# Performance work log

Measured on AMD Instinct MI355X. Metric: run time of the kernel, lower is better.

## Reference

```python
import jax, jax.numpy as jnp
import numpy as np
import math

H = 16
D_MODEL = 1024
D_K = D_MODEL // H
B = 4
S = 2048


def setup_inputs() -> dict:
    key = jax.random.key(0)
    ks = jax.random.split(key, 11)
    s_in = 1.0 / math.sqrt(D_MODEL)
    inp = {
        "query": jax.random.normal(ks[0], (B, S, D_MODEL), dtype=jnp.float32),
        "key_": jax.random.normal(ks[1], (B, S, D_MODEL), dtype=jnp.float32),
        "value": jax.random.normal(ks[2], (B, S, D_MODEL), dtype=jnp.float32),
        # stacked per-head projection weights: [h, d_model, d_k]
        "Wq": jax.random.uniform(ks[3], (H, D_MODEL, D_K), jnp.float32, -s_in, s_in),
        "bq": jax.random.uniform(ks[4], (H, D_K), jnp.float32, -s_in, s_in),
        "Wk": jax.random.uniform(ks[5], (H, D_MODEL, D_K), jnp.float32, -s_in, s_in),
        "bk": jax.random.uniform(ks[6], (H, D_K), jnp.float32, -s_in, s_in),
        "Wv": jax.random.uniform(ks[7], (H, D_MODEL, D_K), jnp.float32, -s_in, s_in),
        "bv": jax.random.uniform(ks[8], (H, D_K), jnp.float32, -s_in, s_in),
        "Wo": jax.random.uniform(ks[9], (D_MODEL, D_MODEL), jnp.float32, -s_in, s_in),
        "bo": jax.random.uniform(ks[10], (D_MODEL,), jnp.float32, -s_in, s_in),
    }
    return inp


def reference(query, key_, value, Wq, bq, Wk, bk, Wv, bv, Wo, bo):
    # Per-head projections, batched over heads: [b,s,m] x [h,m,k] -> [b,h,s,k]
    q = jnp.einsum("bsm,hmk->bhsk", query, Wq) + bq[None, :, None, :]
    k = jnp.einsum("bsm,hmk->bhsk", key_, Wk) + bk[None, :, None, :]
    v = jnp.einsum("bsm,hmk->bhsk", value, Wv) + bv[None, :, None, :]
    # scores: q @ k^T -> [b,h,Sq,Sk]
    scores = jnp.einsum("bhqk,bhsk->bhqs", q, k) / jnp.sqrt(jnp.float32(D_K))
    # NOTE: original code softmaxes over dim=1 of the per-head [N,Sq,Sk]
    # tensor, i.e. the QUERY axis (axis=2 here). Mask has no effect
    # (masked_fill result is discarded in the source), so it is omitted.
    attn = jax.nn.softmax(scores, axis=2)
    ctx = jnp.einsum("bhqs,bhsk->bhqk", attn, v)  # [b,h,Sq,d_k]
    # concat heads along last dim (head-major order matches torch.cat)
    ctx = jnp.transpose(ctx, (0, 2, 1, 3)).reshape(B, S, D_MODEL)
    out = ctx @ Wo.T + bo  # final_W; dropout = identity (eval mode)
    return out
```

## Files before the change

kernel.cpp:

```cpp
#include <hip/hip_runtime.h>


#define DEV __device__ __forceinline__

typedef __bf16 bf16x8 __attribute__((ext_vector_type(8)));
typedef float  f32x4  __attribute__((ext_vector_type(4)));

DEV unsigned short f2bf(float f) {
    __bf16 h = (__bf16)f;
    return __builtin_bit_cast(unsigned short, h);
}

DEV bf16x8 ldfrag(const unsigned short* p) {
    return *reinterpret_cast<const bf16x8*>(p);
}

DEV float fast_exp2(float x) {
#if __has_builtin(__builtin_amdgcn_exp2f)
    return __builtin_amdgcn_exp2f(x);
#else
    return exp2f(x);
#endif
}

DEV void gld16(const unsigned short* g, unsigned short* l) {
    __builtin_amdgcn_global_load_lds(
        (__attribute__((address_space(1))) void*)g,
        (__attribute__((address_space(3))) void*)l, 16, 0, 0);
}

#define MFMA(a,b,c) __builtin_amdgcn_mfma_f32_16x16x32_bf16((a),(b),(c),0,0,0)

#define QSCALE 0.18033688011112042f

__global__ __launch_bounds__(256) void wprep(const float* __restrict__ Wq,
                                             const float* __restrict__ Wk,
                                             const float* __restrict__ Wv,
                                             const float* __restrict__ Wo,
                                             unsigned short* __restrict__ Wt,
                                             unsigned short* __restrict__ Wot) {
    int idx = blockIdx.x * 256 + threadIdx.x;
    int which = blockIdx.y;
    if (which == 3) { Wot[idx] = f2bf(Wo[idx]); return; }
    const float* W = (which == 0) ? Wq : (which == 1) ? Wk : Wv;
    int n = idx >> 10, m = idx & 1023;
    int h = n >> 6, k = n & 63;
    Wt[(size_t)which * 1048576 + idx] = f2bf(W[h * 65536 + m * 64 + k]);
}

__global__ __launch_bounds__(256) void xprep(const float* __restrict__ X,
                                             unsigned short* __restrict__ Xb) {
    int idx = (blockIdx.x * 256 + threadIdx.x) * 4;
    float4 f = *(const float4*)&X[idx];
    ushort4 o;
    o.x = f2bf(f.x); o.y = f2bf(f.y); o.z = f2bf(f.z); o.w = f2bf(f.w);
    *(ushort4*)&Xb[idx] = o;
}

__global__ __launch_bounds__(256) void proj_gemm(
        const unsigned short* __restrict__ Xb, const unsigned short* __restrict__ Bt,
        const float* __restrict__ bias, unsigned short* __restrict__ O,
        unsigned short* __restrict__ Vt, int z) {
    const int tid = threadIdx.x;
    const int bm = blockIdx.x, bn = blockIdx.y;

    __shared__ __align__(16) unsigned short As[128 * 32];
    __shared__ __align__(16) unsigned short Bs[128 * 32];

    const int lane = tid & 63, wid = tid >> 6;
    const int l16 = lane & 15, quad = lane >> 4;
    const int wm = wid & 1, wn = wid >> 1;

    const unsigned short* ga =
        Xb + (size_t)(bm * 128 + wid * 32 + (lane >> 2)) * 1024 + (lane & 3) * 8;
    const unsigned short* gb =
        Bt + (size_t)(bn * 128 + wid * 32 + (lane >> 2)) * 1024 + (lane & 3) * 8;
    unsigned short* la = &As[wid * 32 * 32];
    unsigned short* lb = &Bs[wid * 32 * 32];

    f32x4 acc[4][4] = {};
    for (int kt = 0; kt < 32; ++kt) {
        __syncthreads();
        const int k0 = kt * 32;
        gld16(ga + k0, la);
        gld16(ga + k0 + 16 * 1024, la + 16 * 32);
        gld16(gb + k0, lb);
        gld16(gb + k0 + 16 * 1024, lb + 16 * 32);
        __syncthreads();
        bf16x8 af[4], bfr[4];
#pragma unroll
        for (int mi = 0; mi < 4; ++mi)
            af[mi] = ldfrag(&As[(wm * 64 + mi * 16 + l16) * 32 + quad * 8]);
#pragma unroll
        for (int ni = 0; ni < 4; ++ni)
            bfr[ni] = ldfrag(&Bs[(wn * 64 + ni * 16 + l16) * 32 + quad * 8]);
#pragma unroll
        for (int mi = 0; mi < 4; ++mi)
#pragma unroll
            for (int ni = 0; ni < 4; ++ni)
                acc[mi][ni] = MFMA(af[mi], bfr[ni], acc[mi][ni]);
    }

    if (z == 2) {
#pragma unroll
        for (int mi = 0; mi < 4; ++mi) {
            int row0 = bm * 128 + wm * 64 + mi * 16 + quad * 4;
            int b = row0 >> 11, s0 = row0 & 2047;
#pragma unroll
            for (int ni = 0; ni < 4; ++ni) {
                int col = bn * 128 + wn * 64 + ni * 16 + l16;
                int h = col >> 6, k = col & 63;
                float bi = bias[col];
                ushort4 o;
                o.x = f2bf(acc[mi][ni][0] + bi);
                o.y = f2bf(acc[mi][ni][1] + bi);
                o.z = f2bf(acc[mi][ni][2] + bi);
                o.w = f2bf(acc[mi][ni][3] + bi);
                *(ushort4*)&Vt[(size_t)((b * 16 + h) * 64 + k) * 2048 + s0] = o;
            }
        }
    } else {
#pragma unroll
        for (int mi = 0; mi < 4; ++mi)
#pragma unroll
            for (int ni = 0; ni < 4; ++ni)
#pragma unroll
                for (int r = 0; r < 4; ++r) {
                    int row = bm * 128 + wm * 64 + mi * 16 + quad * 4 + r;
                    int col = bn * 128 + wn * 64 + ni * 16 + l16;
                    float v = acc[mi][ni][r] + bias[col];
                    if (z == 0) v *= QSCALE;
                    int b = row >> 11, s = row & 2047;
                    int h = col >> 6, k = col & 63;
                    O[(size_t)((b * 16 + h) * 2048 + s) * 64 + k] = f2bf(v);
                }
    }
}

__global__ __launch_bounds__(256) void colsum_vscale(
        const unsigned short* __restrict__ Qh, const unsigned short* __restrict__ Kh,
        unsigned short* __restrict__ Vt) {
    const int tid = threadIdx.x;
    const int st = blockIdx.x, bh = blockIdx.y;
    const unsigned short* Qb = Qh + (size_t)bh * 2048 * 64;
    const unsigned short* Kb = Kh + (size_t)bh * 2048 * 64;

    __shared__ __align__(16) unsigned short Qs[2][128 * 64];
    __shared__ float Dtmp[2][128];
    __shared__ float Dsh[128];

    const int lane = tid & 63, wid = tid >> 6;
    const int l16 = lane & 15, quad = lane >> 4;
    const int wm = wid & 1, wn = wid >> 1;
    const int l7 = l16 & 7;

    bf16x8 kf[2][4];
#pragma unroll
    for (int ks = 0; ks < 2; ++ks)
#pragma unroll
        for (int ni = 0; ni < 4; ++ni)
            kf[ks][ni] = ldfrag(&Kb[(size_t)(st * 128 + wn * 64 + ni * 16 + l16) * 64 +
                                    ks * 32 + quad * 8]);

    const unsigned short* gq = Qb + (size_t)(wid * 32 + (lane >> 3)) * 64 +
                               ((lane & 7) ^ (lane >> 3)) * 8;

#pragma unroll
    for (int gi = 0; gi < 4; ++gi)
        gld16(gq + (size_t)gi * 8 * 64, &Qs[0][(wid * 32 + gi * 8) * 64]);

    float psum[4] = {0.f, 0.f, 0.f, 0.f};
    for (int it = 0; it < 16; ++it) {
        const int buf = it & 1;
        __syncthreads();
        if (it < 15) {
            const size_t q1 = (size_t)(it + 1) * 128;
#pragma unroll
            for (int gi = 0; gi < 4; ++gi)
                gld16(gq + (q1 + gi * 8) * 64, &Qs[buf ^ 1][(wid * 32 + gi * 8) * 64]);
        }
        f32x4 acc[4][4] = {};
#pragma unroll
        for (int ks = 0; ks < 2; ++ks) {
            bf16x8 af[4];
#pragma unroll
            for (int mi = 0; mi < 4; ++mi)
                af[mi] = ldfrag(&Qs[buf][(wm * 64 + mi * 16 + l16) * 64 +
                                         (((ks * 4 + quad) ^ l7) * 8)]);
            __builtin_amdgcn_s_setprio(1);
#pragma unroll
            for (int mi = 0; mi < 4; ++mi)
#pragma unroll
                for (int ni = 0; ni < 4; ++ni)
                    acc[mi][ni] = MFMA(af[mi], kf[ks][ni], acc[mi][ni]);
            __builtin_amdgcn_s_setprio(0);
        }
#pragma unroll
        for (int ni = 0; ni < 4; ++ni) {
            float d = 0.f;
#pragma unroll
            for (int mi = 0; mi < 4; ++mi)
#pragma unroll
                for (int r = 0; r < 4; ++r)
                    d += fast_exp2(acc[mi][ni][r]);
            psum[ni] += d;
        }
    }
#pragma unroll
    for (int ni = 0; ni < 4; ++ni) {
        float v = psum[ni];
        v += __shfl_xor(v, 16, 64);
        v += __shfl_xor(v, 32, 64);
        if (quad == 0) Dtmp[wm][wn * 64 + ni * 16 + l16] = v;
    }
    __syncthreads();
    if (tid < 128) Dsh[tid] = 1.0f / (Dtmp[0][tid] + Dtmp[1][tid]);
    __syncthreads();

    const int k = tid >> 2, c = tid & 3;
    unsigned short* vrow = Vt + ((size_t)bh * 64 + k) * 2048 + st * 128 + c * 32;
#pragma unroll
    for (int j = 0; j < 4; ++j) {
        bf16x8 v = *(const bf16x8*)&vrow[j * 8];
        bf16x8 o;
#pragma unroll
        for (int e = 0; e < 8; ++e)
            o[e] = (__bf16)((float)v[e] * Dsh[c * 32 + j * 8 + e]);
        *(bf16x8*)&vrow[j * 8] = o;
    }
}

__global__ __launch_bounds__(256) void attnpv(const unsigned short* __restrict__ Qh,
                                              const unsigned short* __restrict__ Kh,
                                              const unsigned short* __restrict__ Vn,
                                              unsigned short* __restrict__ Ctx) {
    const int tid = threadIdx.x;
    const int qt = blockIdx.x, bh = blockIdx.y;
    const int b = bh >> 4, h = bh & 15;
    const unsigned short* Qb = Qh + (size_t)bh * 2048 * 64;
    const unsigned short* Kb = Kh + (size_t)bh * 2048 * 64;
    const unsigned short* Vb = Vn + (size_t)bh * 64 * 2048;

    __shared__ __align__(16) unsigned char smem[36864];
    unsigned short* Ks = (unsigned short*)smem;
    unsigned short* Vs = (unsigned short*)(smem + 16384);
    unsigned short* Pw = (unsigned short*)(smem + 32768) + (tid >> 6) * 512;

    const int lane = tid & 63, wid = tid >> 6;
    const int l16 = lane & 15, quad = lane >> 4;
    const int wq = wid & 1, ws = wid >> 1;
    const int l7 = l16 & 7;
    const int ph = (l16 >> 1) & 7;
    const int pql = l16 & 1;

    bf16x8 qf[2][4];
#pragma unroll
    for (int ks = 0; ks < 2; ++ks)
#pragma unroll
        for (int nj = 0; nj < 4; ++nj)
            qf[ks][nj] = ldfrag(&Qb[(size_t)(qt * 128 + wq * 64 + nj * 16 + l16) * 64 +
                                    ks * 32 + quad * 8]);

    const int half = wid & 1;
    const int sr8 = lane >> 3;
    const int sg = ((lane & 7) ^ sr8) * 8;
    const unsigned short* gk = Kb + (size_t)(half * 32 + sr8) * 64 + sg;
    const unsigned short* gv = Vb + (size_t)(half * 32 + sr8) * 2048 + sg;

    if (wid < 2) {
#pragma unroll
        for (int gi = 0; gi < 4; ++gi)
            gld16(gk + (size_t)gi * 8 * 64, &Ks[(half * 32 + gi * 8) * 64]);
    } else {
#pragma unroll
        for (int gi = 0; gi < 4; ++gi)
            gld16(gv + (size_t)gi * 8 * 2048, &Vs[(half * 32 + gi * 8) * 64]);
    }

    f32x4 cacc[4][4] = {};
    for (int it = 0; it < 32; ++it) {
        const int pb = it & 1;
        __syncthreads();

        if (it < 31) {
            const size_t s1 = (size_t)(it + 1) * 64;
            if (wid < 2) {
#pragma unroll
                for (int gi = 0; gi < 4; ++gi)
                    gld16(gk + (s1 + gi * 8) * 64,
                          &Ks[(pb ^ 1) * 4096 + (half * 32 + gi * 8) * 64]);
            } else {
#pragma unroll
                for (int gi = 0; gi < 4; ++gi)
                    gld16(gv + (size_t)gi * 8 * 2048 + s1,
                          &Vs[(pb ^ 1) * 4096 + (half * 32 + gi * 8) * 64]);
            }
        }

        bf16x8 kf[2][2];
#pragma unroll
        for (int mi = 0; mi < 2; ++mi)
#pragma unroll
            for (int ks = 0; ks < 2; ++ks)
                kf[mi][ks] = ldfrag(&Ks[pb * 4096 + (ws * 32 + mi * 16 + l16) * 64 +
                                        (((ks * 4 + quad) ^ l7) * 8)]);
        f32x4 sacc[2][4] = {};
        __builtin_amdgcn_s_setprio(1);
#pragma unroll
        for (int ks = 0; ks < 2; ++ks)
#pragma unroll
            for (int mi = 0; mi < 2; ++mi)
#pragma unroll
                for (int nj = 0; nj < 4; ++nj)
                    sacc[mi][nj] = MFMA(kf[mi][ks], qf[ks][nj], sacc[mi][nj]);
        __builtin_amdgcn_s_setprio(0);

        bf16x8 vf[4];
#pragma unroll
        for (int mi = 0; mi < 4; ++mi)
            vf[mi] = ldfrag(&Vs[pb * 4096 + (mi * 16 + l16) * 64 +
                                (((ws * 4 + quad) ^ l7) * 8)]);

#pragma unroll
        for (int nj = 0; nj < 4; ++nj) {
#pragma unroll
            for (int mi = 0; mi < 2; ++mi) {
                const int G = pql * 4 + mi * 2 + (quad >> 1);
                const int po = ((G ^ ph) * 8) + (quad & 1) * 4;
                ushort4 p;
                p.x = f2bf(fast_exp2(sacc[mi][nj][0]));
                p.y = f2bf(fast_exp2(sacc[mi][nj][1]));
                p.z = f2bf(fast_exp2(sacc[mi][nj][2]));
                p.w = f2bf(fast_exp2(sacc[mi][nj][3]));
                *(ushort4*)&Pw[(l16 >> 1) * 64 + po] = p;
            }
            bf16x8 pf = ldfrag(&Pw[(l16 >> 1) * 64 +
                                   (((pql * 4 + quad) ^ ph) * 8)]);
            __builtin_amdgcn_s_setprio(1);
#pragma unroll
            for (int mi = 0; mi < 4; ++mi)
                cacc[mi][nj] = MFMA(vf[mi], pf, cacc[mi][nj]);
            __builtin_amdgcn_s_setprio(0);
        }
    }

    __syncthreads();
    f32x4* Red = (f32x4*)smem;
    if (ws == 1) {
#pragma unroll
        for (int mi = 0; mi < 4; ++mi)
#pragma unroll
            for (int nj = 0; nj < 4; ++nj)
                Red[(wq * 16 + mi * 4 + nj) * 64 + lane] = cacc[mi][nj];
    }
    __syncthreads();
    if (ws == 0) {
#pragma unroll
        for (int mi = 0; mi < 4; ++mi)
#pragma unroll
            for (int nj = 0; nj < 4; ++nj) {
                f32x4 t = Red[(wq * 16 + mi * 4 + nj) * 64 + lane];
                int q = qt * 128 + wq * 64 + nj * 16 + l16;
                int k = mi * 16 + quad * 4;
                ushort4 o;
                o.x = f2bf(cacc[mi][nj][0] + t[0]);
                o.y = f2bf(cacc[mi][nj][1] + t[1]);
                o.z = f2bf(cacc[mi][nj][2] + t[2]);
                o.w = f2bf(cacc[mi][nj][3] + t[3]);
                *(ushort4*)&Ctx[(size_t)(b * 2048 + q) * 1024 + h * 64 + k] = o;
            }
    }
}

__global__ __launch_bounds__(256) void out_gemm(const unsigned short* __restrict__ A,
                                                const unsigned short* __restrict__ Bt,
                                                const float* __restrict__ bias,
                                                float* __restrict__ Out) {
    const int tid = threadIdx.x;
    const int bm = blockIdx.x, bn = blockIdx.y;

    __shared__ __align__(16) unsigned short As[128 * 32];
    __shared__ __align__(16) unsigned short Bs[128 * 32];

    const int lane = tid & 63, wid = tid >> 6;
    const int l16 = lane & 15, quad = lane >> 4;
    const int wm = wid & 1, wn = wid >> 1;

    const unsigned short* ga =
        A + (size_t)(bm * 128 + wid * 32 + (lane >> 2)) * 1024 + (lane & 3) * 8;
    const unsigned short* gb =
        Bt + (size_t)(bn * 128 + wid * 32 + (lane >> 2)) * 1024 + (lane & 3) * 8;
    unsigned short* la = &As[wid * 32 * 32];
    unsigned short* lb = &Bs[wid * 32 * 32];

    f32x4 acc[4][4] = {};
    for (int kt = 0; kt < 32; ++kt) {
        __syncthreads();
        const int k0 = kt * 32;
        gld16(ga + k0, la);
        gld16(ga + k0 + 16 * 1024, la + 16 * 32);
        gld16(gb + k0, lb);
        gld16(gb + k0 + 16 * 1024, lb + 16 * 32);
        __syncthreads();
        bf16x8 af[4], bfr[4];
#pragma unroll
        for (int mi = 0; mi < 4; ++mi)
            af[mi] = ldfrag(&As[(wm * 64 + mi * 16 + l16) * 32 + quad * 8]);
#pragma unroll
        for (int ni = 0; ni < 4; ++ni)
            bfr[ni] = ldfrag(&Bs[(wn * 64 + ni * 16 + l16) * 32 + quad * 8]);
#pragma unroll
        for (int mi = 0; mi < 4; ++mi)
#pragma unroll
            for (int ni = 0; ni < 4; ++ni)
                acc[mi][ni] = MFMA(af[mi], bfr[ni], acc[mi][ni]);
    }
#pragma unroll
    for (int mi = 0; mi < 4; ++mi)
#pragma unroll
        for (int ni = 0; ni < 4; ++ni)
#pragma unroll
            for (int r = 0; r < 4; ++r) {
                int row = bm * 128 + wm * 64 + mi * 16 + quad * 4 + r;
                int col = bn * 128 + wn * 64 + ni * 16 + l16;
                Out[(size_t)row * 1024 + col] = acc[mi][ni][r] + bias[col];
            }
}

extern "C" void kernel_launch(void* const* d_in, const int* in_sizes, int n_in,
                              void* d_out, int out_size, void* d_ws, size_t ws_size,
                              hipStream_t stream) {
    (void)in_sizes; (void)n_in; (void)out_size; (void)ws_size;
    const float* X[3] = {(const float*)d_in[0], (const float*)d_in[1],
                         (const float*)d_in[2]};
    const float* Wq = (const float*)d_in[3];
    const float* bq = (const float*)d_in[4];
    const float* Wk = (const float*)d_in[5];
    const float* bk = (const float*)d_in[6];
    const float* Wv = (const float*)d_in[7];
    const float* bv = (const float*)d_in[8];
    const float* Wo = (const float*)d_in[9];
    const float* bo = (const float*)d_in[10];
    const float* bias[3] = {bq, bk, bv};
    float* Out = (float*)d_out;

    char* ws = (char*)d_ws;
    const size_t MB = 1024 * 1024;
    unsigned short* Wt  = (unsigned short*)(ws);
    unsigned short* Wot = (unsigned short*)(ws + 6 * MB);
    unsigned short* Qh  = (unsigned short*)(ws + 8 * MB);
    unsigned short* Kh  = (unsigned short*)(ws + 24 * MB);
    unsigned short* Vt  = (unsigned short*)(ws + 40 * MB);
    unsigned short* Ctx = (unsigned short*)(ws + 56 * MB);
    unsigned short* Xb  = Ctx;
    unsigned short* Oz[3] = {Qh, Kh, Qh };

    wprep<<<dim3(4096, 4), dim3(256), 0, stream>>>(Wq, Wk, Wv, Wo, Wt, Wot);
    for (int z = 0; z < 3; ++z) {
        xprep<<<dim3(8192), dim3(256), 0, stream>>>(X[z], Xb);
        proj_gemm<<<dim3(64, 8), dim3(256), 0, stream>>>(
            Xb, Wt + (size_t)z * 1048576, bias[z], Oz[z], Vt, z);
    }
    colsum_vscale<<<dim3(16, 64), dim3(256), 0, stream>>>(Qh, Kh, Vt);
    attnpv<<<dim3(16, 64), dim3(256), 0, stream>>>(Qh, Kh, Vt, Ctx);
    out_gemm<<<dim3(64, 8), dim3(256), 0, stream>>>(Ctx, Wot, bo, Out);
}
```

Before: 433.1 us.

## Fuse fp32-to-bf16 input conversion into projection GEMM and batch P staging

The separate xprep kernel is removed. proj_gemm now loads fp32 activations straight into LDS with an XOR swizzle and converts them to bf16 when it builds fragments, which saves one full write and re-read of a bf16 copy per input. In attnpv, all four P tiles are written to a larger per-wave LDS buffer before a single batched MFMA block, instead of interleaving exp, store, load and MFMA per column. The cost is twice the A-tile LDS traffic in the GEMM, and attention LDS grows from 36 KB to 48 KB, which may lower occupancy.

```diff
diff --git a/kernel.cpp b/kernel.cpp
--- a/kernel.cpp
+++ b/kernel.cpp
@@ -23,7 +23,7 @@
 #endif
 }
 
-DEV void gld16(const unsigned short* g, unsigned short* l) {
+DEV void gld16(const void* g, void* l) {
     __builtin_amdgcn_global_load_lds(
         (__attribute__((address_space(1))) void*)g,
         (__attribute__((address_space(3))) void*)l, 16, 0, 0);
@@ -48,49 +48,51 @@
     Wt[(size_t)which * 1048576 + idx] = f2bf(W[h * 65536 + m * 64 + k]);
 }
 
-__global__ __launch_bounds__(256) void xprep(const float* __restrict__ X,
-                                             unsigned short* __restrict__ Xb) {
-    int idx = (blockIdx.x * 256 + threadIdx.x) * 4;
-    float4 f = *(const float4*)&X[idx];
-    ushort4 o;
-    o.x = f2bf(f.x); o.y = f2bf(f.y); o.z = f2bf(f.z); o.w = f2bf(f.w);
-    *(ushort4*)&Xb[idx] = o;
-}
-
 __global__ __launch_bounds__(256) void proj_gemm(
-        const unsigned short* __restrict__ Xb, const unsigned short* __restrict__ Bt,
+        const float* __restrict__ Xf, const unsigned short* __restrict__ Bt,
         const float* __restrict__ bias, unsigned short* __restrict__ O,
         unsigned short* __restrict__ Vt, int z) {
     const int tid = threadIdx.x;
     const int bm = blockIdx.x, bn = blockIdx.y;
 
-    __shared__ __align__(16) unsigned short As[128 * 32];
+    __shared__ __align__(16) float          Asf[128 * 32];
     __shared__ __align__(16) unsigned short Bs[128 * 32];
 
     const int lane = tid & 63, wid = tid >> 6;
     const int l16 = lane & 15, quad = lane >> 4;
     const int wm = wid & 1, wn = wid >> 1;
-
-    const unsigned short* ga =
-        Xb + (size_t)(bm * 128 + wid * 32 + (lane >> 2)) * 1024 + (lane & 3) * 8;
+    const int l7 = l16 & 7;
+
+    const int sr8 = lane >> 3;
+    const float* ga = Xf + (size_t)(bm * 128 + wid * 32 + sr8) * 1024 +
+                      ((lane & 7) ^ sr8) * 4;
     const unsigned short* gb =
         Bt + (size_t)(bn * 128 + wid * 32 + (lane >> 2)) * 1024 + (lane & 3) * 8;
-    unsigned short* la = &As[wid * 32 * 32];
     unsigned short* lb = &Bs[wid * 32 * 32];
 
     f32x4 acc[4][4] = {};
     for (int kt = 0; kt < 32; ++kt) {
         __syncthreads();
         const int k0 = kt * 32;
-        gld16(ga + k0, la);
-        gld16(ga + k0 + 16 * 1024, la + 16 * 32);
+#pragma unroll
+        for (int gi = 0; gi < 4; ++gi)
+            gld16(ga + k0 + (size_t)gi * 8 * 1024, &Asf[(wid * 32 + gi * 8) * 32]);
         gld16(gb + k0, lb);
         gld16(gb + k0 + 16 * 1024, lb + 16 * 32);
         __syncthreads();
         bf16x8 af[4], bfr[4];
 #pragma unroll
-        for (int mi = 0; mi < 4; ++mi)
-            af[mi] = ldfrag(&As[(wm * 64 + mi * 16 + l16) * 32 + quad * 8]);
+        for (int mi = 0; mi < 4; ++mi) {
+            const int r = wm * 64 + mi * 16 + l16;
+            f32x4 a0 = *(const f32x4*)&Asf[r * 32 + (((quad * 2) ^ l7) * 4)];
+            f32x4 a1 = *(const f32x4*)&Asf[r * 32 + (((quad * 2 + 1) ^ l7) * 4)];
+            bf16x8 v;
+            v[0] = (__bf16)a0[0]; v[1] = (__bf16)a0[1];
+            v[2] = (__bf16)a0[2]; v[3] = (__bf16)a0[3];
+            v[4] = (__bf16)a1[0]; v[5] = (__bf16)a1[1];
+            v[6] = (__bf16)a1[2]; v[7] = (__bf16)a1[3];
+            af[mi] = v;
+        }
 #pragma unroll
         for (int ni = 0; ni < 4; ++ni)
             bfr[ni] = ldfrag(&Bs[(wn * 64 + ni * 16 + l16) * 32 + quad * 8]);
@@ -241,10 +243,10 @@
     const unsigned short* Kb = Kh + (size_t)bh * 2048 * 64;
     const unsigned short* Vb = Vn + (size_t)bh * 64 * 2048;
 
-    __shared__ __align__(16) unsigned char smem[36864];
+    __shared__ __align__(16) unsigned char smem[49152];
     unsigned short* Ks = (unsigned short*)smem;
     unsigned short* Vs = (unsigned short*)(smem + 16384);
-    unsigned short* Pw = (unsigned short*)(smem + 32768) + (tid >> 6) * 512;
+    unsigned short* Pw = (unsigned short*)(smem + 32768) + (tid >> 6) * 2048;
 
     const int lane = tid & 63, wid = tid >> 6;
     const int l16 = lane & 15, quad = lane >> 4;
@@ -315,33 +317,37 @@
                     sacc[mi][nj] = MFMA(kf[mi][ks], qf[ks][nj], sacc[mi][nj]);
         __builtin_amdgcn_s_setprio(0);
 
-        bf16x8 vf[4];
-#pragma unroll
-        for (int mi = 0; mi < 4; ++mi)
-            vf[mi] = ldfrag(&Vs[pb * 4096 + (mi * 16 + l16) * 64 +
-                                (((ws * 4 + quad) ^ l7) * 8)]);
-
-#pragma unroll
-        for (int nj = 0; nj < 4; ++nj) {
-#pragma unroll
-            for (int mi = 0; mi < 2; ++mi) {
-                const int G = pql * 4 + mi * 2 + (quad >> 1);
-                const int po = ((G ^ ph) * 8) + (quad & 1) * 4;
+#pragma unroll
+        for (int mi = 0; mi < 2; ++mi) {
+            const int G = pql * 4 + mi * 2 + (quad >> 1);
+            const int po = ((G ^ ph) * 8) + (quad & 1) * 4;
+#pragma unroll
+            for (int nj = 0; nj < 4; ++nj) {
                 ushort4 p;
                 p.x = f2bf(fast_exp2(sacc[mi][nj][0]));
                 p.y = f2bf(fast_exp2(sacc[mi][nj][1]));
                 p.z = f2bf(fast_exp2(sacc[mi][nj][2]));
                 p.w = f2bf(fast_exp2(sacc[mi][nj][3]));
-                *(ushort4*)&Pw[(l16 >> 1) * 64 + po] = p;
+                *(ushort4*)&Pw[(nj * 8 + (l16 >> 1)) * 64 + po] = p;
             }
-            bf16x8 pf = ldfrag(&Pw[(l16 >> 1) * 64 +
-                                   (((pql * 4 + quad) ^ ph) * 8)]);
-            __builtin_amdgcn_s_setprio(1);
-#pragma unroll
-            for (int mi = 0; mi < 4; ++mi)
-                cacc[mi][nj] = MFMA(vf[mi], pf, cacc[mi][nj]);
-            __builtin_amdgcn_s_setprio(0);
-        }
+        }
+
+        bf16x8 vf[4], pf[4];
+#pragma unroll
+        for (int mi = 0; mi < 4; ++mi)
+            vf[mi] = ldfrag(&Vs[pb * 4096 + (mi * 16 + l16) * 64 +
+                                (((ws * 4 + quad) ^ l7) * 8)]);
+#pragma unroll
+        for (int nj = 0; nj < 4; ++nj)
+            pf[nj] = ldfrag(&Pw[(nj * 8 + (l16 >> 1)) * 64 +
+                                (((pql * 4 + quad) ^ ph) * 8)]);
+        __builtin_amdgcn_s_setprio(1);
+#pragma unroll
+        for (int mi = 0; mi < 4; ++mi)
+#pragma unroll
+            for (int nj = 0; nj < 4; ++nj)
+                cacc[mi][nj] = MFMA(vf[mi], pf[nj], cacc[mi][nj]);
+        __builtin_amdgcn_s_setprio(0);
     }
 
     __syncthreads();
@@ -452,14 +458,12 @@
     unsigned short* Kh  = (unsigned short*)(ws + 24 * MB);
     unsigned short* Vt  = (unsigned short*)(ws + 40 * MB);
     unsigned short* Ctx = (unsigned short*)(ws + 56 * MB);
-    unsigned short* Xb  = Ctx;
     unsigned short* Oz[3] = {Qh, Kh, Qh };
 
     wprep<<<dim3(4096, 4), dim3(256), 0, stream>>>(Wq, Wk, Wv, Wo, Wt, Wot);
     for (int z = 0; z < 3; ++z) {
-        xprep<<<dim3(8192), dim3(256), 0, stream>>>(X[z], Xb);
         proj_gemm<<<dim3(64, 8), dim3(256), 0, stream>>>(
-            Xb, Wt + (size_t)z * 1048576, bias[z], Oz[z], Vt, z);
+            X[z], Wt + (size_t)z * 1048576, bias[z], Oz[z], Vt, z);
     }
     colsum_vscale<<<dim3(16, 64), dim3(256), 0, stream>>>(Qh, Kh, Vt);
     attnpv<<<dim3(16, 64), dim3(256), 0, stream>>>(Qh, Kh, Vt, Ctx);
```

New measurement: 437.5 us. No clear change (+1.0%).
